# Optimization experiments

Measured on AMD Instinct MI355X. Metric: run time of the kernel, lower is better.

The kernel has to match this reference:

```python
import jax, jax.numpy as jnp
import numpy as np

# RasterConfig constants (from init_kwargs)
H, W = 128, 128
G = 2048
ALPHA_THR = 1.0 / 255.0          # meta_f32[0]
T_THR = 1e-4                     # meta_f32[1] transmittance_threshold
ALPHA_MAX = 0.99                 # meta_f32[6] alpha clamp
BG = jnp.array([0.0, 0.0, 0.0], dtype=jnp.float32)  # meta_f32[2:5]


def setup_inputs() -> dict:
    key = jax.random.key(0)
    k = jax.random.split(key, 7)
    # gaussian centers spread over the image (in pixel coords)
    means2d = jax.random.uniform(k[0], (G, 2), dtype=jnp.float32) * jnp.array([W, H], dtype=jnp.float32)
    # build positive-definite conics = inverse of random 2D covariances
    sx = jax.random.uniform(k[1], (G,), minval=1.0, maxval=8.0, dtype=jnp.float32)
    sy = jax.random.uniform(k[2], (G,), minval=1.0, maxval=8.0, dtype=jnp.float32)
    rho = jax.random.uniform(k[3], (G,), minval=-0.7, maxval=0.7, dtype=jnp.float32)
    sxx, syy, sxy = sx * sx, sy * sy, rho * sx * sy
    det = sxx * syy - sxy * sxy
    conics = jnp.stack([syy / det, -sxy / det, sxx / det], axis=1).astype(jnp.float32)  # (a,b,c)
    colors = jax.random.uniform(k[4], (G, 3), dtype=jnp.float32)
    opacities = jax.random.uniform(k[5], (G,), minval=0.05, maxval=0.95, dtype=jnp.float32)
    depths = jax.random.uniform(k[6], (G,), minval=0.1, maxval=10.0, dtype=jnp.float32)
    return {"means2d": means2d, "conics": conics, "colors": colors,
            "opacities": opacities, "depths": depths}


def reference(means2d, conics, colors, opacities, depths):
    # depth sort, front-to-back (torch.argsort ascending, stable)
    order = jnp.argsort(depths, stable=True)
    m = means2d[order]            # [G,2]
    con = conics[order]           # [G,3] -> (a,b,c)
    col = colors[order]           # [G,3]
    op = opacities[order]         # [G]

    # pixel centers
    xs = jnp.arange(W, dtype=jnp.float32) + 0.5
    ys = jnp.arange(H, dtype=jnp.float32) + 0.5
    gy, gx = jnp.meshgrid(ys, xs, indexing='ij')
    px = gx.reshape(-1)           # [P], P = H*W
    py = gy.reshape(-1)

    dx = px[:, None] - m[None, :, 0]   # [P,G]
    dy = py[:, None] - m[None, :, 1]
    a, b, c = con[:, 0], con[:, 1], con[:, 2]
    # 0.5 * d^T Sigma^{-1} d with conic (a,b,c)
    sigma = 0.5 * (a * dx * dx + c * dy * dy) + b * dx * dy
    alpha = jnp.minimum(op * jnp.exp(-sigma), ALPHA_MAX)
    # skip invalid quadratic form and sub-threshold alphas
    alpha = jnp.where((sigma < 0.0) | (alpha < ALPHA_THR), 0.0, alpha)

    one_m = 1.0 - alpha
    cp = jnp.cumprod(one_m, axis=1)
    T_before = jnp.concatenate(
        [jnp.ones((px.shape[0], 1), jnp.float32), cp[:, :-1]], axis=1)  # exclusive cumprod
    # early-termination: a gaussian whose inclusion would push T below threshold
    # (and all subsequent ones) is skipped. Terminated set is a suffix since T is
    # monotone nonincreasing, so T_before is exact on the surviving prefix.
    valid = (T_before * one_m) >= T_THR
    w = jnp.where(valid, alpha, 0.0) * T_before     # [P,G] compositing weights
    rgb = w @ col                                    # [P,3]
    final_T = jnp.prod(jnp.where(valid, one_m, 1.0), axis=1)
    img = rgb + final_T[:, None] * BG
    return img.reshape(H, W, 3)
```

## Files before the change

kernel.cpp:

```cpp
#include <hip/hip_runtime.h>
#include <hip/hip_bf16.h>

#define G_COUNT 2048
#define IMG_W 128
#define T_THR 1e-4f
#define ALPHA_MAX 0.99f
#define LOG2E 1.4426950408889634f

__device__ __forceinline__ float fexp2(float x) {
#if __has_builtin(__builtin_amdgcn_exp2f)
    return __builtin_amdgcn_exp2f(x);
#else
    return __expf(x * 0.6931471805599453f);
#endif
}

__device__ __forceinline__ float frcp(float x) {
#if __has_builtin(__builtin_amdgcn_rcpf)
    return __builtin_amdgcn_rcpf(x);
#else
    return 1.0f / x;
#endif
}

__device__ __forceinline__ float clampf(float x, float lo, float hi) {
    return fminf(fmaxf(x, lo), hi);
}

__global__ __launch_bounds__(512)
void raster_fused(const float* __restrict__ means2d,
                  const float* __restrict__ conics,
                  const float* __restrict__ colors,
                  const float* __restrict__ opac,
                  const float* __restrict__ depths,
                  float* __restrict__ out) {
    __shared__ float4 s_r0[G_COUNT + 1];
    __shared__ float4 s_r1[G_COUNT + 1];
    __shared__ float2 s_r2[G_COUNT + 1];
    __shared__ unsigned long long s_key[G_COUNT];
    __shared__ int s_perm[G_COUNT];
    __shared__ float s_T[2][8][64];
    __shared__ float s_rgb[8][192];
    __shared__ int s_cnt;

    const int tid = threadIdx.x;
    const int wv = tid >> 6;
    const int lane = tid & 63;
    const int tile = blockIdx.x;
    const int tx = tile & 15;
    const int ty = tile >> 4;

    if (tid == 0) s_cnt = 0;
    __syncthreads();

    const float bx0 = (float)(tx * 8) + 0.5f;
    const float bx1 = (float)(tx * 8 + 7) + 0.5f;
    const float by0 = (float)(ty * 8) + 0.5f;
    const float by1 = (float)(ty * 8 + 7) + 0.5f;

    for (int k = 0; k < G_COUNT; k += 512) {
        int gi = k + tid;
        float2 m = ((const float2*)means2d)[gi];
        float a = conics[3 * gi + 0];
        float b = conics[3 * gi + 1];
        float c = conics[3 * gi + 2];
        float o = opac[gi];
        float d = depths[gi];

        float A = 0.5f * a * LOG2E;
        float C = 0.5f * c * LOG2E;
        float B = b * LOG2E;
        float l2o = __log2f(255.0f * o);

        float lx = bx0 - m.x, hx = bx1 - m.x;
        float ly = by0 - m.y, hy = by1 - m.y;
        bool inside = (lx <= 0.0f) & (hx >= 0.0f) & (ly <= 0.0f) & (hy >= 0.0f);
        float rC = frcp(C), rA = frcp(A);
        float d1 = clampf(-0.5f * B * lx * rC, ly, hy);
        float d2 = clampf(-0.5f * B * hx * rC, ly, hy);
        float d3 = clampf(-0.5f * B * ly * rA, lx, hx);
        float d4 = clampf(-0.5f * B * hy * rA, lx, hx);
        float m1 = fmaf(A * lx, lx, fmaf(C * d1, d1, (B * lx) * d1));
        float m2 = fmaf(A * hx, hx, fmaf(C * d2, d2, (B * hx) * d2));
        float m3 = fmaf(A * d3, d3, fmaf(C * ly, ly, (B * d3) * ly));
        float m4 = fmaf(A * d4, d4, fmaf(C * hy, hy, (B * d4) * hy));
        float minv = fminf(fminf(m1, m2), fminf(m3, m4));
        bool pass = inside || (minv <= l2o + 0.01f);

        unsigned long long msk = __ballot(pass);
        int prefix = __builtin_amdgcn_mbcnt_hi((unsigned)(msk >> 32),
                     __builtin_amdgcn_mbcnt_lo((unsigned)msk, 0));
        int wbase = 0;
        if (lane == 0) wbase = atomicAdd(&s_cnt, __popcll(msk));
        wbase = __shfl(wbase, 0);
        if (pass) {
            int pos = wbase + prefix;
            s_r0[pos] = make_float4(m.x, m.y, A, C);
            s_r1[pos] = make_float4(B,
                                    colors[3 * gi + 0],
                                    colors[3 * gi + 1],
                                    colors[3 * gi + 2]);
            s_r2[pos] = make_float2(o, l2o);
            s_key[pos] = ((unsigned long long)__float_as_uint(d) << 32) | (unsigned)gi;
        }
    }
    __syncthreads();

    const int n = s_cnt;
    const int npad = (n + 63) & ~63;
    for (int s = tid; s < n; s += 512) {
        unsigned long long key = s_key[s];
        int rk = 0;
#pragma unroll 4
        for (int j = 0; j < n; ++j) {
            rk += (s_key[j] < key) ? 1 : 0;
        }
        s_perm[rk] = s;
    }
    for (int i = n + tid; i < npad; i += 512) s_perm[i] = n;
    if (tid == 0 && n < G_COUNT) {
        s_r0[n] = make_float4(0.f, 0.f, 0.f, 0.f);
        s_r1[n] = make_float4(0.f, 0.f, 0.f, 0.f);
        s_r2[n] = make_float2(0.f, -1.f);
    }
    __syncthreads();

    const int pxi = tx * 8 + (lane & 7);
    const int pyi = ty * 8 + (lane >> 3);
    const float px = (float)pxi + 0.5f;
    const float py = (float)pyi + 0.5f;

    float T = 1.0f;
    float accr = 0.0f, accg = 0.0f, accb = 0.0f;
    const int ngroups = npad >> 6;

    for (int g = 0; g < ngroups; ++g) {
        const int base = g * 64 + wv * 8;
        int pidx[8];
        float4 r0[8], r1[8];
        float2 o2[8];
#pragma unroll
        for (int j = 0; j < 8; ++j) pidx[j] = s_perm[base + j];
#pragma unroll
        for (int j = 0; j < 8; ++j) {
            r0[j] = s_r0[pidx[j]];
            r1[j] = s_r1[pidx[j]];
            o2[j] = s_r2[pidx[j]];
        }
        float al[8], cum[8];
        float run = 1.0f;
#pragma unroll
        for (int j = 0; j < 8; ++j) {
            float dx = px - r0[j].x;
            float dy = py - r0[j].y;
            float s2 = fmaf(r0[j].z * dx, dx, fmaf(r0[j].w * dy, dy, (r1[j].x * dx) * dy));
            float a = fminf(o2[j].x * fexp2(-s2), ALPHA_MAX);
            a = (s2 < 0.0f || s2 > o2[j].y) ? 0.0f : a;
            al[j] = a;
            run *= 1.0f - a;
            cum[j] = run;
        }
        s_T[g & 1][wv][lane] = run;
        __syncthreads();

        float pre = 1.0f, full = 1.0f;
#pragma unroll
        for (int t = 0; t < 8; ++t) {
            float v = s_T[g & 1][t][lane];
            full *= v;
            if (t < wv) pre *= v;
        }
        float Tw0 = T * pre;
#pragma unroll
        for (int j = 0; j < 8; ++j) {
            float Tb = Tw0 * ((j == 0) ? 1.0f : cum[j - 1]);
            float Tn = Tw0 * cum[j];
            float w = (Tn >= T_THR) ? al[j] * Tb : 0.0f;
            accr = fmaf(w, r1[j].y, accr);
            accg = fmaf(w, r1[j].z, accg);
            accb = fmaf(w, r1[j].w, accb);
        }
        T *= full;
        if (__ballot(T >= T_THR) == 0ULL) break;
    }

    s_rgb[wv][lane * 3 + 0] = accr;
    s_rgb[wv][lane * 3 + 1] = accg;
    s_rgb[wv][lane * 3 + 2] = accb;
    __syncthreads();

    if (tid < 192) {
        float sum = 0.0f;
#pragma unroll
        for (int w = 0; w < 8; ++w) sum += s_rgb[w][tid];
        int p2 = tid / 3;
        int ch = tid - p2 * 3;
        int opx = tx * 8 + (p2 & 7);
        int opy = ty * 8 + (p2 >> 3);
        out[((size_t)opy * IMG_W + opx) * 3 + ch] = sum;
    }
}

extern "C" void kernel_launch(void* const* d_in, const int* in_sizes, int n_in,
                              void* d_out, int out_size, void* d_ws, size_t ws_size,
                              hipStream_t stream) {
    const float* means2d = (const float*)d_in[0];
    const float* conics  = (const float*)d_in[1];
    const float* colors  = (const float*)d_in[2];
    const float* opac    = (const float*)d_in[3];
    const float* depths  = (const float*)d_in[4];
    float* out = (float*)d_out;

    raster_fused<<<256, 512, 0, stream>>>(means2d, conics, colors, opac, depths, out);
}
```

Before: 14.48 us.

## Pack gaussian records into two float4s with fp16 colors and vectorize loads

Merges the three per-gaussian shared arrays into two interleaved float4 records, storing colors as half2 so opacity and log2-opacity fit in the record. Alpha is computed as exp2(l2o - s2)/255 instead of o*exp2(-s2). The rank sort reads keys in 128-bit pairs with sentinel padding, and permutation indices are loaded as int4. The aim is fewer LDS instructions per gaussian in the compositing and sort loops, at the cost of fp16 color precision and a slightly different alpha rounding.

```diff
diff --git a/kernel.cpp b/kernel.cpp
--- a/kernel.cpp
+++ b/kernel.cpp
@@ -1,11 +1,13 @@
 #include <hip/hip_runtime.h>
 #include <hip/hip_bf16.h>
+#include <hip/hip_fp16.h>
 
 #define G_COUNT 2048
 #define IMG_W 128
 #define T_THR 1e-4f
 #define ALPHA_MAX 0.99f
 #define LOG2E 1.4426950408889634f
+#define INV255 0.003921568627451f
 
 __device__ __forceinline__ float fexp2(float x) {
 #if __has_builtin(__builtin_amdgcn_exp2f)
@@ -34,11 +36,9 @@
                   const float* __restrict__ opac,
                   const float* __restrict__ depths,
                   float* __restrict__ out) {
-    __shared__ float4 s_r0[G_COUNT + 1];
-    __shared__ float4 s_r1[G_COUNT + 1];
-    __shared__ float2 s_r2[G_COUNT + 1];
-    __shared__ unsigned long long s_key[G_COUNT];
-    __shared__ int s_perm[G_COUNT];
+    __shared__ alignas(16) float4 s_rec[2 * (G_COUNT + 1)];
+    __shared__ alignas(16) unsigned long long s_key[G_COUNT + 2];
+    __shared__ alignas(16) int s_perm[G_COUNT];
     __shared__ float s_T[2][8][64];
     __shared__ float s_rgb[8][192];
     __shared__ int s_cnt;
@@ -95,12 +95,12 @@
         wbase = __shfl(wbase, 0);
         if (pass) {
             int pos = wbase + prefix;
-            s_r0[pos] = make_float4(m.x, m.y, A, C);
-            s_r1[pos] = make_float4(B,
-                                    colors[3 * gi + 0],
-                                    colors[3 * gi + 1],
-                                    colors[3 * gi + 2]);
-            s_r2[pos] = make_float2(o, l2o);
+            __half2 rg = __floats2half2_rn(colors[3 * gi + 0], colors[3 * gi + 1]);
+            __half2 bz = __floats2half2_rn(colors[3 * gi + 2], 0.0f);
+            s_rec[2 * pos + 0] = make_float4(m.x, m.y, A, C);
+            s_rec[2 * pos + 1] = make_float4(B, l2o,
+                                             __uint_as_float(*(unsigned*)&rg),
+                                             __uint_as_float(*(unsigned*)&bz));
             s_key[pos] = ((unsigned long long)__float_as_uint(d) << 32) | (unsigned)gi;
         }
     }
@@ -108,20 +108,25 @@
 
     const int n = s_cnt;
     const int npad = (n + 63) & ~63;
+    if (tid < 2) s_key[n + tid] = ~0ULL;
+    __syncthreads();
+    const int npairs = (n + 1) >> 1;
     for (int s = tid; s < n; s += 512) {
         unsigned long long key = s_key[s];
         int rk = 0;
+        const ulonglong2* kp = (const ulonglong2*)s_key;
 #pragma unroll 4
-        for (int j = 0; j < n; ++j) {
-            rk += (s_key[j] < key) ? 1 : 0;
+        for (int jj = 0; jj < npairs; ++jj) {
+            ulonglong2 k2 = kp[jj];
+            rk += (k2.x < key) ? 1 : 0;
+            rk += (k2.y < key) ? 1 : 0;
         }
         s_perm[rk] = s;
     }
     for (int i = n + tid; i < npad; i += 512) s_perm[i] = n;
     if (tid == 0 && n < G_COUNT) {
-        s_r0[n] = make_float4(0.f, 0.f, 0.f, 0.f);
-        s_r1[n] = make_float4(0.f, 0.f, 0.f, 0.f);
-        s_r2[n] = make_float2(0.f, -1.f);
+        s_rec[2 * n + 0] = make_float4(0.f, 0.f, 0.f, 0.f);
+        s_rec[2 * n + 1] = make_float4(0.f, -1.f, 0.f, 0.f);
     }
     __syncthreads();
 
@@ -136,26 +141,25 @@
 
     for (int g = 0; g < ngroups; ++g) {
         const int base = g * 64 + wv * 8;
-        int pidx[8];
-        float4 r0[8], r1[8];
-        float2 o2[8];
-#pragma unroll
-        for (int j = 0; j < 8; ++j) pidx[j] = s_perm[base + j];
+        const int4* pp4 = (const int4*)(s_perm + base);
+        int4 pa = pp4[0], pb = pp4[1];
+        int pidx[8] = {pa.x, pa.y, pa.z, pa.w, pb.x, pb.y, pb.z, pb.w};
+
+        float4 ra[8], rb[8];
 #pragma unroll
         for (int j = 0; j < 8; ++j) {
-            r0[j] = s_r0[pidx[j]];
-            r1[j] = s_r1[pidx[j]];
-            o2[j] = s_r2[pidx[j]];
+            ra[j] = s_rec[2 * pidx[j] + 0];
+            rb[j] = s_rec[2 * pidx[j] + 1];
         }
         float al[8], cum[8];
         float run = 1.0f;
 #pragma unroll
         for (int j = 0; j < 8; ++j) {
-            float dx = px - r0[j].x;
-            float dy = py - r0[j].y;
-            float s2 = fmaf(r0[j].z * dx, dx, fmaf(r0[j].w * dy, dy, (r1[j].x * dx) * dy));
-            float a = fminf(o2[j].x * fexp2(-s2), ALPHA_MAX);
-            a = (s2 < 0.0f || s2 > o2[j].y) ? 0.0f : a;
+            float dx = px - ra[j].x;
+            float dy = py - ra[j].y;
+            float s2 = fmaf(ra[j].z * dx, dx, fmaf(ra[j].w * dy, dy, (rb[j].x * dx) * dy));
+            float a = fminf(fexp2(rb[j].y - s2) * INV255, ALPHA_MAX);
+            a = (s2 < 0.0f || s2 > rb[j].y) ? 0.0f : a;
             al[j] = a;
             run *= 1.0f - a;
             cum[j] = run;
@@ -176,9 +180,13 @@
             float Tb = Tw0 * ((j == 0) ? 1.0f : cum[j - 1]);
             float Tn = Tw0 * cum[j];
             float w = (Tn >= T_THR) ? al[j] * Tb : 0.0f;
-            accr = fmaf(w, r1[j].y, accr);
-            accg = fmaf(w, r1[j].z, accg);
-            accb = fmaf(w, r1[j].w, accb);
+            unsigned urg = __float_as_uint(rb[j].z);
+            unsigned ub = __float_as_uint(rb[j].w);
+            float2 rg = __half22float2(*(__half2*)&urg);
+            float2 b2 = __half22float2(*(__half2*)&ub);
+            accr = fmaf(w, rg.x, accr);
+            accg = fmaf(w, rg.y, accg);
+            accb = fmaf(w, b2.x, accb);
         }
         T *= full;
         if (__ballot(T >= T_THR) == 0ULL) break;
```

Result: faster. 14.15 us (-2.3%).
